# Kernel optimization log

Measured on AMD Instinct MI355X. Metric: run time of the kernel, lower is better.

Reference implementation:

```python
import jax, jax.numpy as jnp
import numpy as np

LN_EPS = 1e-5


def setup_inputs() -> dict:
    key = jax.random.key(0)
    ks = jax.random.split(key, 4)
    X, Y, F, H, NF = 2048, 256, 128, 8, 32
    xy_feat = jax.random.normal(ks[0], (X, Y, F), dtype=jnp.float32)
    mask = jax.random.randint(ks[1], (X, Y), 0, 2) == 1
    W1 = jax.random.normal(ks[2], (F, H * NF), dtype=jnp.float32) * (1.0 / np.sqrt(F))
    b1 = jnp.zeros((H * NF,), dtype=jnp.float32)
    gamma = jnp.ones((H * NF,), dtype=jnp.float32)
    beta = jnp.zeros((H * NF,), dtype=jnp.float32)
    W2 = jax.random.normal(ks[3], (F, H), dtype=jnp.float32) * (1.0 / np.sqrt(F))
    b2 = jnp.zeros((H,), dtype=jnp.float32)
    return {"xy_feat": xy_feat, "mask": mask, "W1": W1, "b1": b1,
            "gamma": gamma, "beta": beta, "W2": W2, "b2": b2,
            "n_heads": H, "n_feat": NF}


def reference(xy_feat, mask, W1, b1, gamma, beta, W2, b2, n_heads, n_feat):
    X, Y, F = xy_feat.shape
    lr = jax.nn.leaky_relu(xy_feat, negative_slope=0.01)  # shared leaky_relu input
    # NormAndLinear: linear then layernorm over last dim
    hid = jnp.einsum('xyf,fo->xyo', lr, W1) + b1            # (X, Y, H*NF)
    mu = hid.mean(-1, keepdims=True)
    var = hid.var(-1, keepdims=True)
    hn = (hid - mu) * jax.lax.rsqrt(var + LN_EPS) * gamma + beta
    out_feat = hn.reshape(X, Y, n_heads, n_feat)            # (X, Y, H, NF)
    # attention coefficients: linear to H, mask-fill with 0, softmax over Y
    coefs = (jnp.einsum('xyf,fh->xyh', lr, W2) + b2)[..., None]  # (X, Y, H, 1)
    coefs = jnp.where(mask[:, :, None, None], 0.0, coefs)
    coefs = jax.nn.softmax(coefs, axis=-3)                   # softmax over Y
    out = (coefs * out_feat).sum(-3)                         # (X, H, NF)
    return out.reshape(X, n_heads * n_feat)
```

## Files before the change

kernel.cpp:

```cpp
#include <hip/hip_runtime.h>
#include <stdint.h>
#include <stddef.h>


typedef __attribute__((ext_vector_type(8))) _Float16 f16x8;
typedef __attribute__((ext_vector_type(8))) float f32x8;
typedef __attribute__((ext_vector_type(4))) float f32x4;

#define XPB 8
#define NBLK 256

#define OFF_W1   0u
#define OFF_W2   65536u
#define OFF_COEF 69632u
#define OFF_OUTP 77856u
#define OFF_B1   94240u
#define OFF_G    95264u
#define OFF_BT   96288u
#define OFF_B2   97312u
#define LDS_BYTES 97376u

__device__ __forceinline__ f32x4 mfma16(f16x8 a, f16x8 b, f32x4 c){
  return __builtin_amdgcn_mfma_f32_16x16x32_f16(a, b, c, 0, 0, 0);
}

__global__ __launch_bounds__(1024, 4) void attn_main(
    const float* __restrict__ xy, const int* __restrict__ mask,
    const float* __restrict__ W1g, const float* __restrict__ b1g,
    const float* __restrict__ gammag, const float* __restrict__ betag,
    const float* __restrict__ W2g, const float* __restrict__ b2g,
    float* __restrict__ out)
{
  extern __shared__ char smem[];
  const int tid = threadIdx.x;
  const int l  = tid & 63;
  const int w  = tid >> 6;
  const int lg = l >> 4;
  const int lc = l & 15;

  _Float16* w1f = (_Float16*)(smem + OFF_W1);
  _Float16* w2f = (_Float16*)(smem + OFF_W2);
  float* coefT = (float*)(smem + OFF_COEF);
  float* outp  = (float*)(smem + OFF_OUTP);
  float* ldsB1 = (float*)(smem + OFF_B1);
  float* ldsG  = (float*)(smem + OFF_G);
  float* ldsBt = (float*)(smem + OFF_BT);
  float* ldsB2 = (float*)(smem + OFF_B2);

  if (tid < 256){
    ldsB1[tid] = b1g[tid];
    ldsG[tid]  = gammag[tid];
    ldsBt[tid] = betag[tid];
  }
  if (tid < 16) ldsB2[tid] = (tid < 8) ? b2g[tid] : 0.f;

  #pragma unroll
  for (int i = 0; i < 4; ++i){
    int base = i * 8192 + tid * 8;
    int bl  = (base >> 3) & 63;
    int bkk = (base >> 9) & 3;
    int bnt = base >> 11;
    int o   = bnt * 16 + (bl & 15);
    int f0  = bkk * 32 + ((bl >> 4) << 3);
    f16x8 v;
    #pragma unroll
    for (int j = 0; j < 8; ++j) v[j] = (_Float16)W1g[(size_t)(f0 + j) * 256 + o];
    *(f16x8*)(w1f + base) = v;
  }
  if (tid < 256){
    int base = tid * 8;
    int bl  = (base >> 3) & 63;
    int bkk = base >> 9;
    int h   = bl & 15;
    int f0  = bkk * 32 + ((bl >> 4) << 3);
    f16x8 v;
    #pragma unroll
    for (int j = 0; j < 8; ++j)
      v[j] = (h < 8) ? (_Float16)W2g[(size_t)(f0 + j) * 8 + h] : (_Float16)0.f;
    *(f16x8*)(w2f + base) = v;
  }
  __syncthreads();

  const int x0 = blockIdx.x * XPB;

  for (int xi = 0; xi < XPB; ++xi){
    const int x = x0 + xi;

    f32x8 araw[4];
    #pragma unroll
    for (int kk = 0; kk < 4; ++kk)
      araw[kk] = *(const f32x8*)(xy + (((size_t)x * 256 + w * 16 + lc) << 7)
                                    + kk * 32 + (lg << 3));
    int mk[4];
    if (w < 8){
      #pragma unroll
      for (int k = 0; k < 4; ++k) mk[k] = mask[(x << 8) + (k << 6) + l];
    }

    f16x8 ah[4];
    #pragma unroll
    for (int kk = 0; kk < 4; ++kk){
      f32x8 v = araw[kk];
      f16x8 vh;
      #pragma unroll
      for (int j = 0; j < 8; ++j){
        float f = fmaxf(v[j], 0.f) + 0.01f * fminf(v[j], 0.f);
        vh[j] = (_Float16)f;
      }
      ah[kk] = vh;
    }

    {
      f32x4 la = {0.f,0.f,0.f,0.f};
      #pragma unroll
      for (int kk = 0; kk < 4; ++kk){
        f16x8 wb = *(const f16x8*)(w2f + (kk * 64 + l) * 8);
        la = mfma16(ah[kk], wb, la);
      }
      if (lc < 8){
        float b2v = ldsB2[lc];
        #pragma unroll
        for (int r = 0; r < 4; ++r){
          int row = (w << 4) + (lg << 2) + r;
          coefT[lc * 257 + row] = la[r] + b2v;
        }
      }
    }
    __syncthreads();

    if (w < 8){
      float lgv[4];
      #pragma unroll
      for (int k = 0; k < 4; ++k){
        float v = coefT[w * 257 + (k << 6) + l];
        lgv[k] = mk[k] ? 0.f : v;
      }
      float mx = fmaxf(fmaxf(lgv[0], lgv[1]), fmaxf(lgv[2], lgv[3]));
      #pragma unroll
      for (int mm = 1; mm < 64; mm <<= 1) mx = fmaxf(mx, __shfl_xor(mx, mm));
      float e[4]; float sum = 0.f;
      #pragma unroll
      for (int k = 0; k < 4; ++k){ e[k] = __expf(lgv[k] - mx); sum += e[k]; }
      #pragma unroll
      for (int mm = 1; mm < 64; mm <<= 1) sum += __shfl_xor(sum, mm);
      float inv = 1.f / sum;
      #pragma unroll
      for (int k = 0; k < 4; ++k) coefT[w * 257 + (k << 6) + l] = e[k] * inv;
    }

    f32x4 acc[16];
    #pragma unroll
    for (int nt = 0; nt < 16; ++nt) acc[nt] = (f32x4){0.f,0.f,0.f,0.f};

    #pragma unroll
    for (int nt = 0; nt < 16; ++nt){
      #pragma unroll
      for (int kk = 0; kk < 4; ++kk){
        f16x8 b = *(const f16x8*)(w1f + ((nt * 4 + kk) * 64 + l) * 8);
        acc[nt] = mfma16(ah[kk], b, acc[nt]);
      }
    }

    float s[4] = {0.f,0.f,0.f,0.f}, q[4] = {0.f,0.f,0.f,0.f};
    #pragma unroll
    for (int nt = 0; nt < 16; ++nt){
      float bv = ldsB1[nt * 16 + lc];
      #pragma unroll
      for (int r = 0; r < 4; ++r){
        float v = acc[nt][r] + bv;
        acc[nt][r] = v;
        s[r] += v;
        q[r] = fmaf(v, v, q[r]);
      }
    }
    #pragma unroll
    for (int mm = 1; mm <= 8; mm <<= 1){
      #pragma unroll
      for (int r = 0; r < 4; ++r){
        s[r] += __shfl_xor(s[r], mm);
        q[r] += __shfl_xor(q[r], mm);
      }
    }
    float mu[4], rstd[4];
    #pragma unroll
    for (int r = 0; r < 4; ++r){
      float m = s[r] * (1.f / 256.f);
      float var = q[r] * (1.f / 256.f) - m * m;
      mu[r] = m;
      rstd[r] = rsqrtf(fmaxf(var, 0.f) + 1e-5f);
    }
    __syncthreads();

    #pragma unroll
    for (int h = 0; h < 8; ++h){
      float c2[4];
      float Dl = 0.f;
      #pragma unroll
      for (int r = 0; r < 4; ++r){
        float c = coefT[h * 257 + (w << 4) + (lg << 2) + r];
        float v = c * rstd[r];
        c2[r] = v;
        Dl = fmaf(v, mu[r], Dl);
      }
      #pragma unroll
      for (int t = 0; t < 2; ++t){
        int nt = h * 2 + t;
        float p = -Dl;
        #pragma unroll
        for (int r = 0; r < 4; ++r) p = fmaf(c2[r], acc[nt][r], p);
        p += __shfl_xor(p, 16);
        p += __shfl_xor(p, 32);
        if (lg == 0) outp[w * 256 + nt * 16 + lc] = p;
      }
    }
    __syncthreads();

    if (tid < 256){
      float S = 0.f;
      #pragma unroll
      for (int ww = 0; ww < 16; ++ww) S += outp[ww * 256 + tid];
      out[((size_t)x << 8) + tid] = fmaf(ldsG[tid], S, ldsBt[tid]);
    }
  }
}

extern "C" void kernel_launch(void* const* d_in, const int* in_sizes, int n_in,
                              void* d_out, int out_size, void* d_ws, size_t ws_size,
                              hipStream_t stream){
  (void)in_sizes; (void)n_in; (void)out_size; (void)d_ws; (void)ws_size;
  const float* xy    = (const float*)d_in[0];
  const int*   mask  = (const int*)d_in[1];
  const float* W1    = (const float*)d_in[2];
  const float* b1    = (const float*)d_in[3];
  const float* gamma = (const float*)d_in[4];
  const float* beta  = (const float*)d_in[5];
  const float* W2    = (const float*)d_in[6];
  const float* b2    = (const float*)d_in[7];

  hipFuncSetAttribute((const void*)attn_main,
                      hipFuncAttributeMaxDynamicSharedMemorySize, (int)LDS_BYTES);
  attn_main<<<NBLK, 1024, LDS_BYTES, stream>>>(xy, mask, W1, b1, gamma, beta, W2, b2,
                                               (float*)d_out);
}
```

Before: 102.2 us.

## Switch W1 GEMM to 32x32 MFMA tiles with LDS-staged activations

Each wave now computes a 32-row by 128-column tile using 32x32x16 MFMA instead of a 16-row by 256-column tile with 16x16x32 MFMA. This halves the W1 fragment bytes each wave reads from LDS per x row. The f16 leaky-relu activations are written to a new LDS buffer so waves can share rows. Because a row's hidden features are now split across two waves, layernorm sum and sum-of-squares partials are exchanged through LDS. This raises LDS use to about 159KB and changes the layout of the final per-wave output reduction.

```diff
diff --git a/kernel.cpp b/kernel.cpp
--- a/kernel.cpp
+++ b/kernel.cpp
@@ -3,25 +3,31 @@
 #include <stddef.h>
 
 
-typedef __attribute__((ext_vector_type(8))) _Float16 f16x8;
-typedef __attribute__((ext_vector_type(8))) float f32x8;
-typedef __attribute__((ext_vector_type(4))) float f32x4;
+typedef __attribute__((ext_vector_type(8)))  _Float16 f16x8;
+typedef __attribute__((ext_vector_type(8)))  float f32x8;
+typedef __attribute__((ext_vector_type(4)))  float f32x4;
+typedef __attribute__((ext_vector_type(16))) float f32x16;
 
 #define XPB 8
 #define NBLK 256
 
 #define OFF_W1   0u
 #define OFF_W2   65536u
-#define OFF_COEF 69632u
-#define OFF_OUTP 77856u
-#define OFF_B1   94240u
-#define OFF_G    95264u
-#define OFF_BT   96288u
-#define OFF_B2   97312u
-#define LDS_BYTES 97376u
+#define OFF_A    69632u
+#define OFF_COEF 135168u
+#define OFF_OUTP 143392u
+#define OFF_SNQ  151584u
+#define OFF_B1   155680u
+#define OFF_G    156704u
+#define OFF_BT   157728u
+#define OFF_B2   158752u
+#define LDS_BYTES 158816u
 
 __device__ __forceinline__ f32x4 mfma16(f16x8 a, f16x8 b, f32x4 c){
   return __builtin_amdgcn_mfma_f32_16x16x32_f16(a, b, c, 0, 0, 0);
+}
+__device__ __forceinline__ f32x16 mfma32(f16x8 a, f16x8 b, f32x16 c){
+  return __builtin_amdgcn_mfma_f32_32x32x16_f16(a, b, c, 0, 0, 0);
 }
 
 __global__ __launch_bounds__(1024, 4) void attn_main(
@@ -35,13 +41,20 @@
   const int tid = threadIdx.x;
   const int l  = tid & 63;
   const int w  = tid >> 6;
+  const int rg = w >> 1;
+  const int cg = w & 1;
   const int lg = l >> 4;
   const int lc = l & 15;
+  const int c32 = l & 31;
+  const int hi5 = l >> 5;
 
   _Float16* w1f = (_Float16*)(smem + OFF_W1);
   _Float16* w2f = (_Float16*)(smem + OFF_W2);
+  _Float16* af  = (_Float16*)(smem + OFF_A);
   float* coefT = (float*)(smem + OFF_COEF);
   float* outp  = (float*)(smem + OFF_OUTP);
+  float* snqS  = (float*)(smem + OFF_SNQ);
+  float* snqQ  = (float*)(smem + OFF_SNQ + 2048u);
   float* ldsB1 = (float*)(smem + OFF_B1);
   float* ldsG  = (float*)(smem + OFF_G);
   float* ldsBt = (float*)(smem + OFF_BT);
@@ -56,28 +69,28 @@
 
   #pragma unroll
   for (int i = 0; i < 4; ++i){
-    int base = i * 8192 + tid * 8;
-    int bl  = (base >> 3) & 63;
-    int bkk = (base >> 9) & 3;
-    int bnt = base >> 11;
-    int o   = bnt * 16 + (bl & 15);
-    int f0  = bkk * 32 + ((bl >> 4) << 3);
+    int eb = i * 1024 + tid;
+    int bl = eb & 63;
+    int ks = (eb >> 6) & 7;
+    int ct = eb >> 9;
+    int o  = ct * 32 + (bl & 31);
+    int f0 = ks * 16 + ((bl >> 5) << 3);
     f16x8 v;
     #pragma unroll
     for (int j = 0; j < 8; ++j) v[j] = (_Float16)W1g[(size_t)(f0 + j) * 256 + o];
-    *(f16x8*)(w1f + base) = v;
+    *(f16x8*)(w1f + eb * 8) = v;
   }
   if (tid < 256){
-    int base = tid * 8;
-    int bl  = (base >> 3) & 63;
-    int bkk = base >> 9;
+    int eb  = tid;
+    int bl  = eb & 63;
+    int bkk = eb >> 6;
     int h   = bl & 15;
     int f0  = bkk * 32 + ((bl >> 4) << 3);
     f16x8 v;
     #pragma unroll
     for (int j = 0; j < 8; ++j)
       v[j] = (h < 8) ? (_Float16)W2g[(size_t)(f0 + j) * 8 + h] : (_Float16)0.f;
-    *(f16x8*)(w2f + base) = v;
+    *(f16x8*)(w2f + eb * 8) = v;
   }
   __syncthreads();
 
@@ -108,6 +121,8 @@
         vh[j] = (_Float16)f;
       }
       ah[kk] = vh;
+      *(f16x8*)(af + ((((w >> 1) * 8 + 2 * kk + (lg >> 1)) * 64
+                       + 32 * (lg & 1) + 16 * (w & 1) + lc) * 8)) = vh;
     }
 
     {
@@ -148,77 +163,88 @@
       for (int k = 0; k < 4; ++k) coefT[w * 257 + (k << 6) + l] = e[k] * inv;
     }
 
-    f32x4 acc[16];
-    #pragma unroll
-    for (int nt = 0; nt < 16; ++nt) acc[nt] = (f32x4){0.f,0.f,0.f,0.f};
-
-    #pragma unroll
-    for (int nt = 0; nt < 16; ++nt){
-      #pragma unroll
-      for (int kk = 0; kk < 4; ++kk){
-        f16x8 b = *(const f16x8*)(w1f + ((nt * 4 + kk) * 64 + l) * 8);
-        acc[nt] = mfma16(ah[kk], b, acc[nt]);
-      }
-    }
-
-    float s[4] = {0.f,0.f,0.f,0.f}, q[4] = {0.f,0.f,0.f,0.f};
-    #pragma unroll
-    for (int nt = 0; nt < 16; ++nt){
-      float bv = ldsB1[nt * 16 + lc];
-      #pragma unroll
-      for (int r = 0; r < 4; ++r){
-        float v = acc[nt][r] + bv;
-        acc[nt][r] = v;
+    f32x16 acc[4];
+    #pragma unroll
+    for (int ct4 = 0; ct4 < 4; ++ct4)
+      #pragma unroll
+      for (int r = 0; r < 16; ++r) acc[ct4][r] = 0.f;
+
+    #pragma unroll
+    for (int ks = 0; ks < 8; ++ks){
+      f16x8 a = *(const f16x8*)(af + ((rg * 8 + ks) * 64 + l) * 8);
+      #pragma unroll
+      for (int ct4 = 0; ct4 < 4; ++ct4){
+        f16x8 b = *(const f16x8*)(w1f + (((cg * 4 + ct4) * 8 + ks) * 64 + l) * 8);
+        acc[ct4] = mfma32(a, b, acc[ct4]);
+      }
+    }
+
+    float s[16], q[16];
+    #pragma unroll
+    for (int r = 0; r < 16; ++r){ s[r] = 0.f; q[r] = 0.f; }
+    #pragma unroll
+    for (int ct4 = 0; ct4 < 4; ++ct4){
+      float bv = ldsB1[cg * 128 + ct4 * 32 + c32];
+      #pragma unroll
+      for (int r = 0; r < 16; ++r){
+        float v = acc[ct4][r] + bv;
+        acc[ct4][r] = v;
         s[r] += v;
         q[r] = fmaf(v, v, q[r]);
       }
     }
     #pragma unroll
-    for (int mm = 1; mm <= 8; mm <<= 1){
-      #pragma unroll
-      for (int r = 0; r < 4; ++r){
+    for (int mm = 1; mm <= 16; mm <<= 1){
+      #pragma unroll
+      for (int r = 0; r < 16; ++r){
         s[r] += __shfl_xor(s[r], mm);
         q[r] += __shfl_xor(q[r], mm);
       }
     }
-    float mu[4], rstd[4];
-    #pragma unroll
-    for (int r = 0; r < 4; ++r){
-      float m = s[r] * (1.f / 256.f);
-      float var = q[r] * (1.f / 256.f) - m * m;
-      mu[r] = m;
-      rstd[r] = rsqrtf(fmaxf(var, 0.f) + 1e-5f);
+    if (c32 == 0){
+      #pragma unroll
+      for (int r = 0; r < 16; ++r){
+        int row = rg * 32 + (r & 3) + ((r >> 2) << 3) + (hi5 << 2);
+        snqS[row * 2 + cg] = s[r];
+        snqQ[row * 2 + cg] = q[r];
+      }
     }
     __syncthreads();
 
-    #pragma unroll
-    for (int h = 0; h < 8; ++h){
-      float c2[4];
-      float Dl = 0.f;
-      #pragma unroll
-      for (int r = 0; r < 4; ++r){
-        float c = coefT[h * 257 + (w << 4) + (lg << 2) + r];
-        float v = c * rstd[r];
-        c2[r] = v;
-        Dl = fmaf(v, mu[r], Dl);
-      }
-      #pragma unroll
-      for (int t = 0; t < 2; ++t){
-        int nt = h * 2 + t;
-        float p = -Dl;
-        #pragma unroll
-        for (int r = 0; r < 4; ++r) p = fmaf(c2[r], acc[nt][r], p);
-        p += __shfl_xor(p, 16);
-        p += __shfl_xor(p, 32);
-        if (lg == 0) outp[w * 256 + nt * 16 + lc] = p;
-      }
+    float rs16[16], nmz[16];
+    #pragma unroll
+    for (int r = 0; r < 16; ++r){
+      int row = rg * 32 + (r & 3) + ((r >> 2) << 3) + (hi5 << 2);
+      float st = snqS[row * 2] + snqS[row * 2 + 1];
+      float qt = snqQ[row * 2] + snqQ[row * 2 + 1];
+      float m = st * (1.f / 256.f);
+      float var = qt * (1.f / 256.f) - m * m;
+      float rs = rsqrtf(fmaxf(var, 0.f) + 1e-5f);
+      rs16[r] = rs;
+      nmz[r]  = -rs * m;
+    }
+
+    #pragma unroll
+    for (int ct4 = 0; ct4 < 4; ++ct4){
+      int h = cg * 4 + ct4;
+      float p = 0.f;
+      #pragma unroll
+      for (int r = 0; r < 16; ++r){
+        int row = rg * 32 + (r & 3) + ((r >> 2) << 3) + (hi5 << 2);
+        float c = coefT[h * 257 + row];
+        float t = fmaf(rs16[r], acc[ct4][r], nmz[r]);
+        p = fmaf(c, t, p);
+      }
+      p += __shfl_xor(p, 32);
+      if (l < 32) outp[w * 128 + ct4 * 32 + c32] = p;
     }
     __syncthreads();
 
     if (tid < 256){
+      int cgc = tid >> 7, ci = tid & 127;
       float S = 0.f;
       #pragma unroll
-      for (int ww = 0; ww < 16; ++ww) S += outp[ww * 256 + tid];
+      for (int r8 = 0; r8 < 8; ++r8) S += outp[(r8 * 2 + cgc) * 128 + ci];
       out[((size_t)x << 8) + tid] = fmaf(ldsG[tid], S, ldsBt[tid]);
     }
   }
```

Measured after the change: 341.8 us. +234.5%, slower.

## Split block into two wave groups ping-ponging load/logits and GEMM phases

Applied to the files above, without the earlier changes.

The 16 waves are split into two groups of 8, each owning its own coefficient and partial-output LDS buffers. Each group handles one x row in two 128-row halves, and the groups alternate so that one converts inputs and computes logits while the other runs the W1 GEMM and LayerNorm reduction. The aim is to overlap global memory loads with MFMA work, which used to be serialized across the whole block. In exchange each wave does twice the per-row work in sequence, LDS use grows, and barriers are still block-wide, so the overlap depends on phase lengths being balanced.

```diff
diff --git a/kernel.cpp b/kernel.cpp
--- a/kernel.cpp
+++ b/kernel.cpp
@@ -10,15 +10,17 @@
 #define XPB 8
 #define NBLK 256
 
-#define OFF_W1   0u
-#define OFF_W2   65536u
-#define OFF_COEF 69632u
-#define OFF_OUTP 77856u
-#define OFF_B1   94240u
-#define OFF_G    95264u
-#define OFF_BT   96288u
-#define OFF_B2   97312u
-#define LDS_BYTES 97376u
+#define OFF_W1    0u
+#define OFF_W2    65536u
+#define OFF_COEF0 69632u
+#define OFF_COEF1 77856u
+#define OFF_OUTP0 86080u
+#define OFF_OUTP1 94272u
+#define OFF_B1    102464u
+#define OFF_G     103488u
+#define OFF_BT    104512u
+#define OFF_B2    105536u
+#define LDS_BYTES 105600u
 
 __device__ __forceinline__ f32x4 mfma16(f16x8 a, f16x8 b, f32x4 c){
   return __builtin_amdgcn_mfma_f32_16x16x32_f16(a, b, c, 0, 0, 0);
@@ -35,13 +37,15 @@
   const int tid = threadIdx.x;
   const int l  = tid & 63;
   const int w  = tid >> 6;
+  const int g  = w >> 3;
+  const int wg = w & 7;
   const int lg = l >> 4;
   const int lc = l & 15;
 
   _Float16* w1f = (_Float16*)(smem + OFF_W1);
   _Float16* w2f = (_Float16*)(smem + OFF_W2);
-  float* coefT = (float*)(smem + OFF_COEF);
-  float* outp  = (float*)(smem + OFF_OUTP);
+  float* coefT = (float*)(smem + (g ? OFF_COEF1 : OFF_COEF0));
+  float* outp  = (float*)(smem + (g ? OFF_OUTP1 : OFF_OUTP0));
   float* ldsB1 = (float*)(smem + OFF_B1);
   float* ldsG  = (float*)(smem + OFF_G);
   float* ldsBt = (float*)(smem + OFF_BT);
@@ -83,24 +87,14 @@
 
   const int x0 = blockIdx.x * XPB;
 
-  for (int xi = 0; xi < XPB; ++xi){
-    const int x = x0 + xi;
-
-    f32x8 araw[4];
-    #pragma unroll
-    for (int kk = 0; kk < 4; ++kk)
-      araw[kk] = *(const f32x8*)(xy + (((size_t)x * 256 + w * 16 + lc) << 7)
-                                    + kk * 32 + (lg << 3));
-    int mk[4];
-    if (w < 8){
-      #pragma unroll
-      for (int k = 0; k < 4; ++k) mk[k] = mask[(x << 8) + (k << 6) + l];
-    }
-
-    f16x8 ah[4];
+  f16x8 ah1[4], ah2[4];
+  int mk[4];
+
+  auto CONV = [&](int x, int half, f16x8* ah){
     #pragma unroll
     for (int kk = 0; kk < 4; ++kk){
-      f32x8 v = araw[kk];
+      f32x8 v = *(const f32x8*)(xy + (((size_t)x * 256 + half * 128 + wg * 16 + lc) << 7)
+                                   + kk * 32 + (lg << 3));
       f16x8 vh;
       #pragma unroll
       for (int j = 0; j < 8; ++j){
@@ -109,49 +103,50 @@
       }
       ah[kk] = vh;
     }
-
-    {
-      f32x4 la = {0.f,0.f,0.f,0.f};
-      #pragma unroll
-      for (int kk = 0; kk < 4; ++kk){
-        f16x8 wb = *(const f16x8*)(w2f + (kk * 64 + l) * 8);
-        la = mfma16(ah[kk], wb, la);
-      }
-      if (lc < 8){
-        float b2v = ldsB2[lc];
-        #pragma unroll
-        for (int r = 0; r < 4; ++r){
-          int row = (w << 4) + (lg << 2) + r;
-          coefT[lc * 257 + row] = la[r] + b2v;
-        }
-      }
-    }
-    __syncthreads();
-
-    if (w < 8){
-      float lgv[4];
-      #pragma unroll
-      for (int k = 0; k < 4; ++k){
-        float v = coefT[w * 257 + (k << 6) + l];
-        lgv[k] = mk[k] ? 0.f : v;
-      }
-      float mx = fmaxf(fmaxf(lgv[0], lgv[1]), fmaxf(lgv[2], lgv[3]));
-      #pragma unroll
-      for (int mm = 1; mm < 64; mm <<= 1) mx = fmaxf(mx, __shfl_xor(mx, mm));
-      float e[4]; float sum = 0.f;
-      #pragma unroll
-      for (int k = 0; k < 4; ++k){ e[k] = __expf(lgv[k] - mx); sum += e[k]; }
-      #pragma unroll
-      for (int mm = 1; mm < 64; mm <<= 1) sum += __shfl_xor(sum, mm);
-      float inv = 1.f / sum;
-      #pragma unroll
-      for (int k = 0; k < 4; ++k) coefT[w * 257 + (k << 6) + l] = e[k] * inv;
-    }
-
+  };
+  auto LOGITS = [&](const f16x8* ah, int half){
+    f32x4 la = {0.f,0.f,0.f,0.f};
+    #pragma unroll
+    for (int kk = 0; kk < 4; ++kk){
+      f16x8 wb = *(const f16x8*)(w2f + (kk * 64 + l) * 8);
+      la = mfma16(ah[kk], wb, la);
+    }
+    if (lc < 8){
+      float b2v = ldsB2[lc];
+      #pragma unroll
+      for (int r = 0; r < 4; ++r){
+        int row = half * 128 + (wg << 4) + (lg << 2) + r;
+        coefT[lc * 257 + row] = la[r] + b2v;
+      }
+    }
+  };
+  auto MASKLD = [&](int x){
+    #pragma unroll
+    for (int k = 0; k < 4; ++k) mk[k] = mask[(x << 8) + (k << 6) + l];
+  };
+  auto SOFTMAX = [&](){
+    float lgv[4];
+    #pragma unroll
+    for (int k = 0; k < 4; ++k){
+      float v = coefT[wg * 257 + (k << 6) + l];
+      lgv[k] = mk[k] ? 0.f : v;
+    }
+    float mx = fmaxf(fmaxf(lgv[0], lgv[1]), fmaxf(lgv[2], lgv[3]));
+    #pragma unroll
+    for (int mm = 1; mm < 64; mm <<= 1) mx = fmaxf(mx, __shfl_xor(mx, mm));
+    float e[4]; float sum = 0.f;
+    #pragma unroll
+    for (int k = 0; k < 4; ++k){ e[k] = __expf(lgv[k] - mx); sum += e[k]; }
+    #pragma unroll
+    for (int mm = 1; mm < 64; mm <<= 1) sum += __shfl_xor(sum, mm);
+    float inv = 1.f / sum;
+    #pragma unroll
+    for (int k = 0; k < 4; ++k) coefT[wg * 257 + (k << 6) + l] = e[k] * inv;
+  };
+  auto GEMMC = [&](const f16x8* ah, int half){
     f32x4 acc[16];
     #pragma unroll
     for (int nt = 0; nt < 16; ++nt) acc[nt] = (f32x4){0.f,0.f,0.f,0.f};
-
     #pragma unroll
     for (int nt = 0; nt < 16; ++nt){
       #pragma unroll
@@ -160,7 +155,6 @@
         acc[nt] = mfma16(ah[kk], b, acc[nt]);
       }
     }
-
     float s[4] = {0.f,0.f,0.f,0.f}, q[4] = {0.f,0.f,0.f,0.f};
     #pragma unroll
     for (int nt = 0; nt < 16; ++nt){
@@ -189,15 +183,13 @@
       mu[r] = m;
       rstd[r] = rsqrtf(fmaxf(var, 0.f) + 1e-5f);
     }
-    __syncthreads();
-
     #pragma unroll
     for (int h = 0; h < 8; ++h){
       float c2[4];
       float Dl = 0.f;
       #pragma unroll
       for (int r = 0; r < 4; ++r){
-        float c = coefT[h * 257 + (w << 4) + (lg << 2) + r];
+        float c = coefT[h * 257 + half * 128 + (wg << 4) + (lg << 2) + r];
         float v = c * rstd[r];
         c2[r] = v;
         Dl = fmaf(v, mu[r], Dl);
@@ -210,18 +202,53 @@
         for (int r = 0; r < 4; ++r) p = fmaf(c2[r], acc[nt][r], p);
         p += __shfl_xor(p, 16);
         p += __shfl_xor(p, 32);
-        if (lg == 0) outp[w * 256 + nt * 16 + lc] = p;
-      }
-    }
-    __syncthreads();
-
-    if (tid < 256){
+        if (lg == 0){
+          int o = wg * 256 + nt * 16 + lc;
+          if (half == 0) outp[o] = p; else outp[o] += p;
+        }
+      }
+    }
+  };
+  auto REDUCE = [&](int x){
+    int t5 = tid & 511;
+    if (t5 < 256){
       float S = 0.f;
       #pragma unroll
-      for (int ww = 0; ww < 16; ++ww) S += outp[ww * 256 + tid];
-      out[((size_t)x << 8) + tid] = fmaf(ldsG[tid], S, ldsBt[tid]);
-    }
-  }
+      for (int ww = 0; ww < 8; ++ww) S += outp[ww * 256 + t5];
+      out[((size_t)x << 8) + t5] = fmaf(ldsG[t5], S, ldsBt[t5]);
+    }
+  };
+
+  #pragma clang loop unroll(disable)
+  for (int i = 0; i < XPB / 2; ++i){
+    const int xe = x0 + 2 * i;
+    const int xo = xe + 1;
+    const int xop = xe - 1;
+
+    if (g == 0){ CONV(xe, 0, ah1); LOGITS(ah1, 0); }
+    else if (i > 0){ GEMMC(ah1, 0); }
+    __syncthreads();
+    if (g == 0){ CONV(xe, 1, ah2); LOGITS(ah2, 1); MASKLD(xe); }
+    else if (i > 0){ GEMMC(ah2, 1); }
+    __syncthreads();
+    if (g == 0){ SOFTMAX(); }
+    else if (i > 0){ REDUCE(xop); }
+    __syncthreads();
+    if (g == 0){ GEMMC(ah1, 0); }
+    else { CONV(xo, 0, ah1); LOGITS(ah1, 0); }
+    __syncthreads();
+    if (g == 0){ GEMMC(ah2, 1); }
+    else { CONV(xo, 1, ah2); LOGITS(ah2, 1); MASKLD(xo); }
+    __syncthreads();
+    if (g == 0){ REDUCE(xe); }
+    else { SOFTMAX(); }
+    __syncthreads();
+  }
+  if (g == 1) GEMMC(ah1, 0);
+  __syncthreads();
+  if (g == 1) GEMMC(ah2, 1);
+  __syncthreads();
+  if (g == 1) REDUCE(x0 + XPB - 1);
 }
 
 extern "C" void kernel_launch(void* const* d_in, const int* in_sizes, int n_in,
```

Result: slower. 126.1 us (+23.4%).
